# Performance work log

Hardware: AMD Instinct MI355X
Metric: run time of the kernel (lower is better)

Reference implementation:

```python
import jax, jax.numpy as jnp
from jax import lax
import numpy as np

GRID = 8
H384 = 6 * GRID * GRID  # 384, LSTM input and hidden size


def _conv(x, w, b):
    # x: [B,C,H,W], w: [O,I,kh,kw]
    y = lax.conv_general_dilated(x, w, (1, 1), 'VALID',
                                 dimension_numbers=('NCHW', 'OIHW', 'NCHW'))
    return y + b[None, :, None, None]


def _maxpool2(x):
    return lax.reduce_window(x, -jnp.inf, lax.max,
                             (1, 1, 2, 2), (1, 1, 2, 2), 'VALID')


def setup_inputs() -> dict:
    key = jax.random.key(0)
    ks = jax.random.split(key, 20)
    s = 0.05
    d = {
        'x': jax.random.normal(ks[0], (512, 100, 100), jnp.float32),
        # conv stack: Conv2d(1,16,7) ... Conv2d(128,128,3)
        'cw1': jax.random.normal(ks[1], (16, 1, 7, 7), jnp.float32) * s,
        'cb1': jnp.zeros((16,), jnp.float32),
        'cw2': jax.random.normal(ks[2], (32, 16, 4, 4), jnp.float32) * s,
        'cb2': jnp.zeros((32,), jnp.float32),
        'cw3': jax.random.normal(ks[3], (64, 32, 5, 5), jnp.float32) * s,
        'cb3': jnp.zeros((64,), jnp.float32),
        'cw4': jax.random.normal(ks[4], (128, 64, 5, 5), jnp.float32) * s,
        'cb4': jnp.zeros((128,), jnp.float32),
        'cw5': jax.random.normal(ks[5], (128, 128, 5, 5), jnp.float32) * s,
        'cb5': jnp.zeros((128,), jnp.float32),
        'cw6': jax.random.normal(ks[6], (128, 128, 3, 3), jnp.float32) * s,
        'cb6': jnp.zeros((128,), jnp.float32),
        # linear layers: 8192 -> 1024 -> 384, Sigmoid
        'lw1': jax.random.normal(ks[7], (1024, 8192), jnp.float32) * 0.01,
        'lb1': jnp.zeros((1024,), jnp.float32),
        'lw2': jax.random.normal(ks[8], (384, 1024), jnp.float32) * 0.02,
        'lb2': jnp.zeros((384,), jnp.float32),
        # LSTM (input 384, hidden 384, 1 layer), torch gate order i,f,g,o
        'w_ih': jax.random.normal(ks[9], (4 * H384, H384), jnp.float32) * s,
        'w_hh': jax.random.normal(ks[10], (4 * H384, H384), jnp.float32) * s,
        'b_ih': jnp.zeros((4 * H384,), jnp.float32),
        'b_hh': jnp.zeros((4 * H384,), jnp.float32),
    }
    return d


def reference(x, cw1, cb1, cw2, cb2, cw3, cb3, cw4, cb4, cw5, cb5, cw6, cb6,
              lw1, lb1, lw2, lb2, w_ih, w_hh, b_ih, b_hh):
    B = x.shape[0]
    h = x[:, None, :, :]                       # [B,1,100,100]
    h = _maxpool2(jax.nn.relu(_conv(h, cw1, cb1)))   # [B,16,47,47]
    h = _maxpool2(jax.nn.relu(_conv(h, cw2, cb2)))   # [B,32,22,22]
    h = jax.nn.relu(_conv(h, cw3, cb3))              # [B,64,18,18]
    h = jax.nn.relu(_conv(h, cw4, cb4))              # [B,128,14,14]
    h = jax.nn.relu(_conv(h, cw5, cb5))              # [B,128,10,10]
    h = jax.nn.relu(_conv(h, cw6, cb6))              # [B,128,8,8]
    h = h.reshape(B, -1)                             # [B,8192]
    h = h @ lw1.T + lb1                              # [B,1024]
    h = jax.nn.sigmoid(h @ lw2.T + lb2)              # [B,384]

    # Sequential LSTM over the batch dim with carried (h,c) state
    def step(carry, xt):
        hs, cs = carry
        gates = w_ih @ xt + b_ih + w_hh @ hs + b_hh  # [1536]
        i, f, g, o = jnp.split(gates, 4)
        cs = jax.nn.sigmoid(f) * cs + jax.nn.sigmoid(i) * jnp.tanh(g)
        hs = jax.nn.sigmoid(o) * jnp.tanh(cs)
        return (hs, cs), hs

    init = (jnp.zeros((H384,), x.dtype), jnp.zeros((H384,), x.dtype))
    _, ys = lax.scan(step, init, h)                  # [B,384]
    return ys.reshape(B, 6, GRID, GRID)
```

## Files before the change

### kernel.cpp

```cpp
#include <hip/hip_runtime.h>
#include <cstddef>
#include <cstdint>

#define T256 256

typedef __attribute__((ext_vector_type(8))) short bhalf8;
typedef __attribute__((ext_vector_type(4))) float floatx4;

__device__ __forceinline__ ushort f2bf(float f) {
  union { float f; uint32_t u; } v; v.f = f;
  return (ushort)((v.u + 0x7fffu + ((v.u >> 16) & 1u)) >> 16);
}

__device__ __forceinline__ float fsig(float x) {
  return 1.f / (1.f + __expf(-x));
}
__device__ __forceinline__ float ftanh(float x) {
  const float e = __expf(-2.f * fabsf(x));
  const float r = (1.f - e) / (1.f + e);
  return copysignf(r, x);
}

__global__ __launch_bounds__(256) void conv1_pool_k(
    const float* __restrict__ x, const float* __restrict__ w,
    const float* __restrict__ bias, float* __restrict__ out)
{
  __shared__ float img[10000];
  __shared__ float wsm[16 * 49];
  __shared__ float bsm[16];
  const int b = blockIdx.x, tid = threadIdx.x;
  for (int i = tid; i < 10000; i += T256) img[i] = x[(size_t)b * 10000 + i];
  for (int i = tid; i < 16 * 49; i += T256) wsm[i] = w[i];
  if (tid < 16) bsm[tid] = bias[tid];
  __syncthreads();
  for (int p = tid; p < 47 * 47; p += T256) {
    const int py = p / 47, px = p % 47;
    const int iy0 = 2 * py, ix0 = 2 * px;
    float win[8][8];
#pragma unroll
    for (int r = 0; r < 8; ++r)
#pragma unroll
      for (int c = 0; c < 8; ++c)
        win[r][c] = img[(iy0 + r) * 100 + (ix0 + c)];
#pragma unroll 1
    for (int oc = 0; oc < 16; ++oc) {
      float wr[49];
#pragma unroll
      for (int j = 0; j < 49; ++j) wr[j] = wsm[oc * 49 + j];
      float m = 0.f;
#pragma unroll
      for (int dy = 0; dy < 2; ++dy)
#pragma unroll
        for (int dx = 0; dx < 2; ++dx) {
          float s = bsm[oc];
#pragma unroll
          for (int ky = 0; ky < 7; ++ky)
#pragma unroll
            for (int kx = 0; kx < 7; ++kx)
              s += win[dy + ky][dx + kx] * wr[ky * 7 + kx];
          m = fmaxf(m, s);
        }
      out[((size_t)b * 16 + oc) * 2209 + p] = m;
    }
  }
}

__device__ __forceinline__ void wprep_one(
    const float* __restrict__ w, ushort* __restrict__ bswz,
    int IC, int KW, int OC, int idx)
{
  const int NT = OC / 16;
  const int lane = idx & 63;
  const int nt = (idx >> 6) % NT;
  const int ks = idx / (64 * NT);
  const int oc = nt * 16 + (lane & 15);
  const int kb = ks * 32 + (lane >> 4) * 8;
  ushort tmp[8];
#pragma unroll
  for (int j = 0; j < 8; ++j) {
    const int k = kb + j;
    const int ic = k % IC, tap = k / IC;
    tmp[j] = f2bf(w[((size_t)oc * IC + ic) * (KW * KW) + tap]);
  }
  *(bhalf8*)(bswz + (size_t)idx * 8) = *(const bhalf8*)tmp;
}

__global__ __launch_bounds__(256) void wprep_all_k(
    const float* __restrict__ cw2, const float* __restrict__ cw3,
    const float* __restrict__ cw4, const float* __restrict__ cw5,
    const float* __restrict__ cw6,
    ushort* __restrict__ bw2, ushort* __restrict__ bw3,
    ushort* __restrict__ bw4, ushort* __restrict__ bw5,
    ushort* __restrict__ bw6)
{
  int idx = blockIdx.x * 256 + threadIdx.x;
  if (idx < 6400)  { wprep_one(cw3, bw3, 32, 5, 64, idx); return; }
  idx -= 6400;
  if (idx < 25600) { wprep_one(cw4, bw4, 64, 5, 128, idx); return; }
  idx -= 25600;
  if (idx < 51200) { wprep_one(cw5, bw5, 128, 5, 128, idx); return; }
  idx -= 51200;
  if (idx < 18432) { wprep_one(cw6, bw6, 128, 3, 128, idx); return; }
  idx -= 18432;
  if (idx < 1024)  { wprep_one(cw2, bw2, 16, 4, 32, idx); }
}

__global__ __launch_bounds__(256) void wprep_lin_k(
    const float* __restrict__ w, ushort* __restrict__ bswz,
    int Kdim, int NT, int total)
{
  const int idx = blockIdx.x * 256 + threadIdx.x;
  if (idx >= total) return;
  const int lane = idx & 63;
  const int nt = (idx >> 6) % NT;
  const int ks = idx / (64 * NT);
  const int oc = nt * 16 + (lane & 15);
  const int kb = ks * 32 + (lane >> 4) * 8;
  ushort tmp[8];
#pragma unroll
  for (int j = 0; j < 8; ++j) tmp[j] = f2bf(w[(size_t)oc * Kdim + kb + j]);
  *(bhalf8*)(bswz + (size_t)idx * 8) = *(const bhalf8*)tmp;
}

__global__ __launch_bounds__(256) void f2bf_k(
    const float* __restrict__ in, ushort* __restrict__ outv, int n)
{
  const int i = (blockIdx.x * 256 + threadIdx.x) * 4;
  if (i >= n) return;
  const float4 v = *(const float4*)&in[i];
  ushort tmp[4] = {f2bf(v.x), f2bf(v.y), f2bf(v.z), f2bf(v.w)};
  *(uint2*)&outv[i] = *(const uint2*)tmp;
}

__global__ __launch_bounds__(256) void conv2mfma_k(
    const float* __restrict__ in, const ushort* __restrict__ bswz,
    const float* __restrict__ bias, float* __restrict__ out)
{
  constexpr int IC = 16, IH = 47, IW = 47;
  constexpr int NPIX = IH * IW;
  constexpr int ROWU = IC + 8;
  constexpr int KS = 8;
  __shared__ ushort imgT[NPIX * ROWU];
  const int b = blockIdx.x, tid = threadIdx.x;
  const int lane = tid & 63, wv = tid >> 6;

  for (int e = tid; e < IC * NPIX; e += 256) {
    const int ic = e / NPIX, pix = e % NPIX;
    imgT[pix * ROWU + ic] = f2bf(in[((size_t)b * IC + ic) * NPIX + pix]);
  }
  __syncthreads();

  const int col = lane & 15, g = lane >> 4;
  const float b0 = bias[col], b1 = bias[16 + col];

  for (int it = wv; it < 66; it += 4) {
    const int pyp = it / 3, tx = it - pyp * 3;
    int px = tx * 16 + col; px = px < 43 ? px : 43;
    floatx4 acc[2][2];
#pragma unroll
    for (int dy = 0; dy < 2; ++dy)
#pragma unroll
      for (int nt = 0; nt < 2; ++nt) acc[dy][nt] = (floatx4){0.f, 0.f, 0.f, 0.f};

    for (int ks = 0; ks < KS; ++ks) {
      bhalf8 bf[2];
#pragma unroll
      for (int nt = 0; nt < 2; ++nt)
        bf[nt] = *(const bhalf8*)(bswz + ((size_t)(ks * 2 + nt) * 64 + lane) * 8);
      const int kk = ks * 32 + g * 8;
      const int tap = kk >> 4, icb = kk & 15;
      const int ky = tap >> 2, kx = tap & 3;
      bhalf8 af[2];
#pragma unroll
      for (int dy = 0; dy < 2; ++dy)
        af[dy] = *(const bhalf8*)&imgT[((2 * pyp + dy + ky) * IW + px + kx) * ROWU + icb];
#pragma unroll
      for (int dy = 0; dy < 2; ++dy)
#pragma unroll
        for (int nt = 0; nt < 2; ++nt)
          acc[dy][nt] = __builtin_amdgcn_mfma_f32_16x16x32_bf16(
              af[dy], bf[nt], acc[dy][nt], 0, 0, 0);
    }
#pragma unroll
    for (int nt = 0; nt < 2; ++nt) {
      const int oc = nt * 16 + col;
      const float bb = nt ? b1 : b0;
      float vv[4];
#pragma unroll
      for (int i = 0; i < 4; ++i) vv[i] = fmaxf(acc[0][nt][i], acc[1][nt][i]);
#pragma unroll
      for (int q = 0; q < 2; ++q) {
        const int pxp = tx * 8 + g * 2 + q;
        if (pxp < 22) {
          const float v = fmaxf(fmaxf(vv[2 * q], vv[2 * q + 1]) + bb, 0.f);
          out[((size_t)b * 32 + oc) * 484 + pyp * 22 + pxp] = v;
        }
      }
    }
  }
}

template <int IC, int IH, int IW, int KW_, int OC, int MC>
__global__ __launch_bounds__(256) void convmfma_k(
    const float* __restrict__ in, const ushort* __restrict__ bswz,
    const float* __restrict__ bias, float* __restrict__ out)
{
  constexpr int OH = IH - KW_ + 1, OW = IW - KW_ + 1, P = OH * OW;
  constexpr int NPIX = IH * IW;
  constexpr int KS = IC * KW_ * KW_ / 32;
  constexpr int NT = OC / 16;
  constexpr int NPW = NT / 4;
  constexpr int MT = (P + 15) / 16;
  constexpr int ROWU = IC + 8;
  static_assert(NT % 4 == 0 && IC % 32 == 0, "cfg");

  __shared__ ushort imgT[NPIX * ROWU];
  const int b = blockIdx.x, tid = threadIdx.x;
  const int lane = tid & 63, wv = tid >> 6;
  const int icoff = (lane >> 4) * 8;

  for (int e = tid; e < IC * NPIX; e += 256) {
    const int ic = e / NPIX, pix = e % NPIX;
    imgT[pix * ROWU + ic] = f2bf(in[((size_t)b * IC + ic) * NPIX + pix]);
  }
  __syncthreads();

  for (int m0 = 0; m0 < MT; m0 += MC) {
    floatx4 acc[MC][NPW];
#pragma unroll
    for (int mi = 0; mi < MC; ++mi)
#pragma unroll
      for (int nn = 0; nn < NPW; ++nn)
        acc[mi][nn] = (floatx4){0.f, 0.f, 0.f, 0.f};

    int pbase[MC];
#pragma unroll
    for (int mi = 0; mi < MC; ++mi) {
      int p = (m0 + mi) * 16 + (lane & 15);
      p = p < P ? p : P - 1;
      pbase[mi] = ((p / OW) * IW + (p % OW)) * ROWU;
    }

    bhalf8 bcur[NPW];
#pragma unroll
    for (int nn = 0; nn < NPW; ++nn)
      bcur[nn] = *(const bhalf8*)(bswz + ((size_t)(wv * NPW + nn) * 64 + lane) * 8);

    for (int ks = 0; ks < KS; ++ks) {
      bhalf8 bnext[NPW];
      if (ks + 1 < KS) {
#pragma unroll
        for (int nn = 0; nn < NPW; ++nn)
          bnext[nn] = *(const bhalf8*)(bswz +
              ((size_t)((ks + 1) * NT + wv * NPW + nn) * 64 + lane) * 8);
      }
      const int tap = (ks * 32) / IC;
      const int icb = (ks * 32) % IC;
      const int aoff = ((tap / KW_) * IW + (tap % KW_)) * ROWU + icb + icoff;
      bhalf8 af[MC];
#pragma unroll
      for (int mi = 0; mi < MC; ++mi)
        af[mi] = *(const bhalf8*)&imgT[pbase[mi] + aoff];
#pragma unroll
      for (int mi = 0; mi < MC; ++mi)
#pragma unroll
        for (int nn = 0; nn < NPW; ++nn)
          acc[mi][nn] = __builtin_amdgcn_mfma_f32_16x16x32_bf16(
              af[mi], bcur[nn], acc[mi][nn], 0, 0, 0);
      if (ks + 1 < KS) {
#pragma unroll
        for (int nn = 0; nn < NPW; ++nn) bcur[nn] = bnext[nn];
      }
    }
#pragma unroll
    for (int mi = 0; mi < MC; ++mi)
#pragma unroll
      for (int nn = 0; nn < NPW; ++nn) {
        const int oc = (wv * NPW + nn) * 16 + (lane & 15);
#pragma unroll
        for (int i = 0; i < 4; ++i) {
          const int p = (m0 + mi) * 16 + (lane >> 4) * 4 + i;
          if (p < P) {
            const float v = fmaxf(acc[mi][nn][i] + bias[oc], 0.f);
            out[((size_t)b * OC + oc) * P + p] = v;
          }
        }
      }
  }
}

__global__ __launch_bounds__(256) void gemm_bf16_k(
    const ushort* __restrict__ abf, const ushort* __restrict__ bswz,
    const float* __restrict__ bias, float* __restrict__ C,
    int M, int N, int K)
{
  __shared__ ushort As[64][72];
  const int bn = blockIdx.x, bm = blockIdx.y, tid = threadIdx.x;
  const int lane = tid & 63, wv = tid >> 6;
  const int m0 = bm * 64, n0 = bn * 64;
  const int NTg = N / 16;
  const int ntg = bn * 4 + wv;
  floatx4 acc[4];
#pragma unroll
  for (int mt = 0; mt < 4; ++mt) acc[mt] = (floatx4){0.f, 0.f, 0.f, 0.f};

  for (int kc = 0; kc < K / 64; ++kc) {
    __syncthreads();
#pragma unroll
    for (int q = 0; q < 2; ++q) {
      const int id = q * 256 + tid;
      const int row = id >> 3, kcol = (id & 7) * 8;
      *(bhalf8*)&As[row][kcol] =
          *(const bhalf8*)&abf[(size_t)(m0 + row) * K + kc * 64 + kcol];
    }
    __syncthreads();
#pragma unroll
    for (int k2 = 0; k2 < 2; ++k2) {
      const int ks = kc * 2 + k2;
      const bhalf8 bf = *(const bhalf8*)(bswz + ((size_t)(ks * NTg + ntg) * 64 + lane) * 8);
      const int ksub = k2 * 32 + (lane >> 4) * 8;
#pragma unroll
      for (int mt = 0; mt < 4; ++mt) {
        const bhalf8 af = *(const bhalf8*)&As[mt * 16 + (lane & 15)][ksub];
        acc[mt] = __builtin_amdgcn_mfma_f32_16x16x32_bf16(af, bf, acc[mt], 0, 0, 0);
      }
    }
  }
  const int n = n0 + wv * 16 + (lane & 15);
  const float bb = bias[n];
#pragma unroll
  for (int mt = 0; mt < 4; ++mt)
#pragma unroll
    for (int i = 0; i < 4; ++i) {
      const int m = m0 + mt * 16 + (lane >> 4) * 4 + i;
      C[(size_t)m * N + n] = acc[mt][i] + bb;
    }
}

template <int ACT>
__global__ __launch_bounds__(256) void gemm_tn_k(
    const float* __restrict__ A, const float* __restrict__ B,
    const float* __restrict__ b1, const float* __restrict__ b2,
    float* __restrict__ C, int M, int N, int K)
{
  __shared__ float As[32][66];
  __shared__ float Bs[32][36];
  const int bn = blockIdx.x, bm = blockIdx.y, tid = threadIdx.x;
  const int tx = tid & 7, ty = tid >> 3;
  const int m0 = bm * 64, n0 = bn * 32;
  double acc[2][4] = {{0, 0, 0, 0}, {0, 0, 0, 0}};
  for (int k0 = 0; k0 < K; k0 += 32) {
    __syncthreads();
#pragma unroll
    for (int l = 0; l < 8; ++l) {
      int id = tid + l * 256;
      int kk = id & 31, mm = id >> 5;
      As[kk][mm] = A[(size_t)(m0 + mm) * K + (k0 + kk)];
    }
#pragma unroll
    for (int l = 0; l < 4; ++l) {
      int id = tid + l * 256;
      int kk = id & 31, nn = id >> 5;
      Bs[kk][nn] = B[(size_t)(n0 + nn) * K + (k0 + kk)];
    }
    __syncthreads();
    float p[2][4] = {{0.f, 0.f, 0.f, 0.f}, {0.f, 0.f, 0.f, 0.f}};
#pragma unroll
    for (int kk = 0; kk < 32; ++kk) {
      const float2 av = *reinterpret_cast<const float2*>(&As[kk][ty * 2]);
      const float4 bv = *reinterpret_cast<const float4*>(&Bs[kk][tx * 4]);
      p[0][0] += av.x * bv.x; p[0][1] += av.x * bv.y;
      p[0][2] += av.x * bv.z; p[0][3] += av.x * bv.w;
      p[1][0] += av.y * bv.x; p[1][1] += av.y * bv.y;
      p[1][2] += av.y * bv.z; p[1][3] += av.y * bv.w;
    }
#pragma unroll
    for (int i = 0; i < 2; ++i)
#pragma unroll
      for (int j = 0; j < 4; ++j) acc[i][j] += (double)p[i][j];
  }
#pragma unroll
  for (int i = 0; i < 2; ++i) {
    const int m = m0 + ty * 2 + i;
#pragma unroll
    for (int j = 0; j < 4; ++j) {
      const int n = n0 + tx * 4 + j;
      double v = acc[i][j] + (double)b1[n];
      if (b2) v += (double)b2[n];
      if (ACT == 1) v = 1.0 / (1.0 + exp(-v));
      C[(size_t)m * N + n] = (float)v;
    }
  }
}

#define NWG 16
#define CPW 24
__global__ __launch_bounds__(768) void lstm_k(
    const float* __restrict__ gin, const float* __restrict__ whh,
    float* __restrict__ out, unsigned long long* __restrict__ tagged)
{
  __shared__ __align__(16) float hsm[8][52];
  __shared__ float gsum[96];
  const int wg = blockIdx.x, tid = threadIdx.x;
  const int r = tid >> 3, lk = tid & 7;
  const int gq = r / CPW, cl = r % CPW;
  const int grow = gq * 384 + wg * CPW + cl;
  float wreg[48];
  {
    const float* wr = whh + (size_t)grow * 384 + lk * 48;
#pragma unroll
    for (int i = 0; i < 48; ++i) wreg[i] = wr[i];
  }
  float c = 0.f;
  if (tid < 64) __builtin_amdgcn_s_setprio(1);
  __syncthreads();
  for (int t = 0; t < 512; ++t) {
    float g0 = 0.f, g1 = 0.f, g2 = 0.f, g3 = 0.f;
    if (tid < CPW) {
      const int j = wg * CPW + tid;
      g0 = gin[(size_t)t * 1536 + 0 * 384 + j];
      g1 = gin[(size_t)t * 1536 + 1 * 384 + j];
      g2 = gin[(size_t)t * 1536 + 2 * 384 + j];
      g3 = gin[(size_t)t * 1536 + 3 * 384 + j];
    }
    if (tid < 384) {
      float hv;
      if (t == 0) {
        hv = 0.f;
      } else {
        unsigned long long u;
        do {
          u = __hip_atomic_load(&tagged[(size_t)(t - 1) * 384 + tid],
                                __ATOMIC_RELAXED, __HIP_MEMORY_SCOPE_AGENT);
        } while ((unsigned)(u >> 32) != (unsigned)t);
        union { unsigned ui; float f; } cv; cv.ui = (unsigned)u; hv = cv.f;
      }
      hsm[tid / 48][tid % 48] = hv;
    }
    __syncthreads();
    float s = 0.f;
    {
      const float4* hp = (const float4*)&hsm[lk][0];
#pragma unroll
      for (int q = 0; q < 12; ++q) {
        const float4 hv = hp[q];
        s += wreg[4 * q + 0] * hv.x + wreg[4 * q + 1] * hv.y
           + wreg[4 * q + 2] * hv.z + wreg[4 * q + 3] * hv.w;
      }
    }
    s += __shfl_xor(s, 1);
    s += __shfl_xor(s, 2);
    s += __shfl_xor(s, 4);
    if (lk == 0) gsum[r] = s;
    __syncthreads();
    if (tid < CPW) {
      const float gi = gsum[0 * CPW + tid] + g0;
      const float gf = gsum[1 * CPW + tid] + g1;
      const float gg = gsum[2 * CPW + tid] + g2;
      const float go = gsum[3 * CPW + tid] + g3;
      const float si = fsig(gi);
      const float sf = fsig(gf);
      const float so = fsig(go);
      c = sf * c + si * ftanh(gg);
      const float hn = so * ftanh(c);
      const int j = wg * CPW + tid;
      union { float f; unsigned ui; } cv; cv.f = hn;
      const unsigned long long pk = ((unsigned long long)(t + 1) << 32) | cv.ui;
      __hip_atomic_store(&tagged[(size_t)t * 384 + j], pk,
                         __ATOMIC_RELAXED, __HIP_MEMORY_SCOPE_AGENT);
      out[(size_t)t * 384 + j] = hn;
    }
  }
}

extern "C" void kernel_launch(void* const* d_in, const int* in_sizes, int n_in,
                              void* d_out, int out_size, void* d_ws, size_t ws_size,
                              hipStream_t stream)
{
  const float* x   = (const float*)d_in[0];
  const float* cw1 = (const float*)d_in[1];
  const float* cb1 = (const float*)d_in[2];
  const float* cw2 = (const float*)d_in[3];
  const float* cb2 = (const float*)d_in[4];
  const float* cw3 = (const float*)d_in[5];
  const float* cb3 = (const float*)d_in[6];
  const float* cw4 = (const float*)d_in[7];
  const float* cb4 = (const float*)d_in[8];
  const float* cw5 = (const float*)d_in[9];
  const float* cb5 = (const float*)d_in[10];
  const float* cw6 = (const float*)d_in[11];
  const float* cb6 = (const float*)d_in[12];
  const float* lw1 = (const float*)d_in[13];
  const float* lb1 = (const float*)d_in[14];
  const float* lw2 = (const float*)d_in[15];
  const float* lb2 = (const float*)d_in[16];
  const float* wih = (const float*)d_in[17];
  const float* whh = (const float*)d_in[18];
  const float* bih = (const float*)d_in[19];
  const float* bhh = (const float*)d_in[20];
  float* out = (float*)d_out;
  char* ws = (char*)d_ws;

  float* bufA = (float*)(ws);
  float* bufB = (float*)(ws + 72384512);
  float* l1o  = (float*)(ws + 123764736);
  float* x2   = (float*)(ws + 125861888);
  float* gin  = (float*)(ws + 126648320);
  ushort* bw3 = (ushort*)(ws + 123764736);
  ushort* bw4 = (ushort*)(ws + 123764736 + 102400);
  ushort* bw5 = (ushort*)(ws + 123764736 + 512000);
  ushort* bw6 = (ushort*)(ws + 123764736 + 1331200);
  ushort* bw2 = (ushort*)(ws + 123764736 + 1626112);
  ushort* bw1 = (ushort*)(ws);
  ushort* abf = (ushort*)(ws + 16777216);
  unsigned long long* tagged = (unsigned long long*)(ws + 25165824);

  wprep_all_k<<<(102656 + 255) / 256, 256, 0, stream>>>(
      cw2, cw3, cw4, cw5, cw6, bw2, bw3, bw4, bw5, bw6);

  conv1_pool_k<<<512, 256, 0, stream>>>(x, cw1, cb1, bufA);
  conv2mfma_k<<<512, 256, 0, stream>>>(bufA, bw2, cb2, bufB);
  convmfma_k<32, 22, 22, 5, 64, 7><<<512, 256, 0, stream>>>(bufB, bw3, cb3, bufA);
  convmfma_k<64, 18, 18, 5, 128, 7><<<512, 256, 0, stream>>>(bufA, bw4, cb4, bufB);
  convmfma_k<128, 14, 14, 5, 128, 7><<<512, 256, 0, stream>>>(bufB, bw5, cb5, bufA);
  convmfma_k<128, 10, 10, 3, 128, 4><<<512, 256, 0, stream>>>(bufA, bw6, cb6, bufB);
  wprep_lin_k<<<(256 * 64 * 64 + 255) / 256, 256, 0, stream>>>(lw1, bw1, 8192, 64, 256 * 64 * 64);
  f2bf_k<<<(512 * 8192 / 4 + 255) / 256, 256, 0, stream>>>(bufB, abf, 512 * 8192);
  hipMemsetAsync(tagged, 0, 512 * 384 * 8, stream);
  gemm_bf16_k<<<dim3(16, 8), 256, 0, stream>>>(abf, bw1, lb1, l1o, 512, 1024, 8192);
  gemm_tn_k<1><<<dim3(384 / 32, 512 / 64), 256, 0, stream>>>(l1o, lw2, lb2, nullptr, x2, 512, 384, 1024);
  gemm_tn_k<0><<<dim3(1536 / 32, 512 / 64), 256, 0, stream>>>(x2, wih, bih, bhh, gin, 512, 1536, 384);
  lstm_k<<<NWG, 768, 0, stream>>>(gin, whh, out, tagged);
}
```

Before: 1.428 ms.

## Move small linear GEMMs to bf16 MFMA and fuse fp32-to-bf16 conversion

Replaces the fp32/double-accumulating SIMT GEMMs for the 1024->384 linear layer and the LSTM input projection with the bf16 MFMA GEMM. Weight swizzling for all three linear weights is merged into one prep kernel. The activation fp32->bf16 conversion moves into the GEMM's shared-memory load, which removes the separate f2bf pass and its intermediate buffer. The LSTM dot product is also split into two accumulators for more ILP. In exchange, these layers now run at bf16 precision where they previously accumulated in double.

```diff
diff --git a/kernel.cpp b/kernel.cpp
--- a/kernel.cpp
+++ b/kernel.cpp
@@ -105,12 +105,10 @@
   if (idx < 1024)  { wprep_one(cw2, bw2, 16, 4, 32, idx); }
 }
 
-__global__ __launch_bounds__(256) void wprep_lin_k(
+__device__ __forceinline__ void wprep_lin_one(
     const float* __restrict__ w, ushort* __restrict__ bswz,
-    int Kdim, int NT, int total)
-{
-  const int idx = blockIdx.x * 256 + threadIdx.x;
-  if (idx >= total) return;
+    int Kdim, int NT, int idx)
+{
   const int lane = idx & 63;
   const int nt = (idx >> 6) % NT;
   const int ks = idx / (64 * NT);
@@ -122,14 +120,18 @@
   *(bhalf8*)(bswz + (size_t)idx * 8) = *(const bhalf8*)tmp;
 }
 
-__global__ __launch_bounds__(256) void f2bf_k(
-    const float* __restrict__ in, ushort* __restrict__ outv, int n)
-{
-  const int i = (blockIdx.x * 256 + threadIdx.x) * 4;
-  if (i >= n) return;
-  const float4 v = *(const float4*)&in[i];
-  ushort tmp[4] = {f2bf(v.x), f2bf(v.y), f2bf(v.z), f2bf(v.w)};
-  *(uint2*)&outv[i] = *(const uint2*)tmp;
+__global__ __launch_bounds__(256) void wprep_lin3_k(
+    const float* __restrict__ lw1, const float* __restrict__ lw2,
+    const float* __restrict__ wih,
+    ushort* __restrict__ bw1, ushort* __restrict__ bwl2,
+    ushort* __restrict__ bwih)
+{
+  int idx = blockIdx.x * 256 + threadIdx.x;
+  if (idx < 1048576) { wprep_lin_one(lw1, bw1, 8192, 64, idx); return; }
+  idx -= 1048576;
+  if (idx < 49152)   { wprep_lin_one(lw2, bwl2, 1024, 24, idx); return; }
+  idx -= 49152;
+  if (idx < 73728)   { wprep_lin_one(wih, bwih, 384, 96, idx); }
 }
 
 __global__ __launch_bounds__(256) void conv2mfma_k(
@@ -289,10 +291,11 @@
   }
 }
 
+template <int ACT>
 __global__ __launch_bounds__(256) void gemm_bf16_k(
-    const ushort* __restrict__ abf, const ushort* __restrict__ bswz,
-    const float* __restrict__ bias, float* __restrict__ C,
-    int M, int N, int K)
+    const float* __restrict__ A, const ushort* __restrict__ bswz,
+    const float* __restrict__ b1, const float* __restrict__ b2,
+    float* __restrict__ C, int M, int N, int K)
 {
   __shared__ ushort As[64][72];
   const int bn = blockIdx.x, bm = blockIdx.y, tid = threadIdx.x;
@@ -310,8 +313,12 @@
     for (int q = 0; q < 2; ++q) {
       const int id = q * 256 + tid;
       const int row = id >> 3, kcol = (id & 7) * 8;
-      *(bhalf8*)&As[row][kcol] =
-          *(const bhalf8*)&abf[(size_t)(m0 + row) * K + kc * 64 + kcol];
+      const float* ap = &A[(size_t)(m0 + row) * K + kc * 64 + kcol];
+      const float4 v0 = *(const float4*)ap;
+      const float4 v1 = *(const float4*)(ap + 4);
+      ushort t[8] = {f2bf(v0.x), f2bf(v0.y), f2bf(v0.z), f2bf(v0.w),
+                     f2bf(v1.x), f2bf(v1.y), f2bf(v1.z), f2bf(v1.w)};
+      *(bhalf8*)&As[row][kcol] = *(const bhalf8*)t;
     }
     __syncthreads();
 #pragma unroll
@@ -327,70 +334,16 @@
     }
   }
   const int n = n0 + wv * 16 + (lane & 15);
-  const float bb = bias[n];
+  const float bb = b1[n] + (b2 ? b2[n] : 0.f);
 #pragma unroll
   for (int mt = 0; mt < 4; ++mt)
 #pragma unroll
     for (int i = 0; i < 4; ++i) {
       const int m = m0 + mt * 16 + (lane >> 4) * 4 + i;
-      C[(size_t)m * N + n] = acc[mt][i] + bb;
-    }
-}
-
-template <int ACT>
-__global__ __launch_bounds__(256) void gemm_tn_k(
-    const float* __restrict__ A, const float* __restrict__ B,
-    const float* __restrict__ b1, const float* __restrict__ b2,
-    float* __restrict__ C, int M, int N, int K)
-{
-  __shared__ float As[32][66];
-  __shared__ float Bs[32][36];
-  const int bn = blockIdx.x, bm = blockIdx.y, tid = threadIdx.x;
-  const int tx = tid & 7, ty = tid >> 3;
-  const int m0 = bm * 64, n0 = bn * 32;
-  double acc[2][4] = {{0, 0, 0, 0}, {0, 0, 0, 0}};
-  for (int k0 = 0; k0 < K; k0 += 32) {
-    __syncthreads();
-#pragma unroll
-    for (int l = 0; l < 8; ++l) {
-      int id = tid + l * 256;
-      int kk = id & 31, mm = id >> 5;
-      As[kk][mm] = A[(size_t)(m0 + mm) * K + (k0 + kk)];
-    }
-#pragma unroll
-    for (int l = 0; l < 4; ++l) {
-      int id = tid + l * 256;
-      int kk = id & 31, nn = id >> 5;
-      Bs[kk][nn] = B[(size_t)(n0 + nn) * K + (k0 + kk)];
-    }
-    __syncthreads();
-    float p[2][4] = {{0.f, 0.f, 0.f, 0.f}, {0.f, 0.f, 0.f, 0.f}};
-#pragma unroll
-    for (int kk = 0; kk < 32; ++kk) {
-      const float2 av = *reinterpret_cast<const float2*>(&As[kk][ty * 2]);
-      const float4 bv = *reinterpret_cast<const float4*>(&Bs[kk][tx * 4]);
-      p[0][0] += av.x * bv.x; p[0][1] += av.x * bv.y;
-      p[0][2] += av.x * bv.z; p[0][3] += av.x * bv.w;
-      p[1][0] += av.y * bv.x; p[1][1] += av.y * bv.y;
-      p[1][2] += av.y * bv.z; p[1][3] += av.y * bv.w;
-    }
-#pragma unroll
-    for (int i = 0; i < 2; ++i)
-#pragma unroll
-      for (int j = 0; j < 4; ++j) acc[i][j] += (double)p[i][j];
-  }
-#pragma unroll
-  for (int i = 0; i < 2; ++i) {
-    const int m = m0 + ty * 2 + i;
-#pragma unroll
-    for (int j = 0; j < 4; ++j) {
-      const int n = n0 + tx * 4 + j;
-      double v = acc[i][j] + (double)b1[n];
-      if (b2) v += (double)b2[n];
-      if (ACT == 1) v = 1.0 / (1.0 + exp(-v));
-      C[(size_t)m * N + n] = (float)v;
-    }
-  }
+      float v = acc[mt][i] + bb;
+      if (ACT == 1) v = 1.f / (1.f + expf(-v));
+      C[(size_t)m * N + n] = v;
+    }
 }
 
 #define NWG 16
@@ -438,16 +391,19 @@
       hsm[tid / 48][tid % 48] = hv;
     }
     __syncthreads();
-    float s = 0.f;
+    float s0 = 0.f, s1 = 0.f;
     {
       const float4* hp = (const float4*)&hsm[lk][0];
 #pragma unroll
-      for (int q = 0; q < 12; ++q) {
-        const float4 hv = hp[q];
-        s += wreg[4 * q + 0] * hv.x + wreg[4 * q + 1] * hv.y
-           + wreg[4 * q + 2] * hv.z + wreg[4 * q + 3] * hv.w;
-      }
-    }
+      for (int q = 0; q < 12; q += 2) {
+        const float4 ha = hp[q], hb = hp[q + 1];
+        s0 += wreg[4 * q + 0] * ha.x + wreg[4 * q + 1] * ha.y
+            + wreg[4 * q + 2] * ha.z + wreg[4 * q + 3] * ha.w;
+        s1 += wreg[4 * q + 4] * hb.x + wreg[4 * q + 5] * hb.y
+            + wreg[4 * q + 6] * hb.z + wreg[4 * q + 7] * hb.w;
+      }
+    }
+    float s = s0 + s1;
     s += __shfl_xor(s, 1);
     s += __shfl_xor(s, 2);
     s += __shfl_xor(s, 4);
@@ -511,9 +467,10 @@
   ushort* bw5 = (ushort*)(ws + 123764736 + 512000);
   ushort* bw6 = (ushort*)(ws + 123764736 + 1331200);
   ushort* bw2 = (ushort*)(ws + 123764736 + 1626112);
-  ushort* bw1 = (ushort*)(ws);
-  ushort* abf = (ushort*)(ws + 16777216);
+  ushort* bw1  = (ushort*)(ws);
   unsigned long long* tagged = (unsigned long long*)(ws + 25165824);
+  ushort* bwl2 = (ushort*)(ws + 26738688);
+  ushort* bwih = (ushort*)(ws + 27525120);
 
   wprep_all_k<<<(102656 + 255) / 256, 256, 0, stream>>>(
       cw2, cw3, cw4, cw5, cw6, bw2, bw3, bw4, bw5, bw6);
@@ -524,11 +481,11 @@
   convmfma_k<64, 18, 18, 5, 128, 7><<<512, 256, 0, stream>>>(bufA, bw4, cb4, bufB);
   convmfma_k<128, 14, 14, 5, 128, 7><<<512, 256, 0, stream>>>(bufB, bw5, cb5, bufA);
   convmfma_k<128, 10, 10, 3, 128, 4><<<512, 256, 0, stream>>>(bufA, bw6, cb6, bufB);
-  wprep_lin_k<<<(256 * 64 * 64 + 255) / 256, 256, 0, stream>>>(lw1, bw1, 8192, 64, 256 * 64 * 64);
-  f2bf_k<<<(512 * 8192 / 4 + 255) / 256, 256, 0, stream>>>(bufB, abf, 512 * 8192);
+  wprep_lin3_k<<<(1171456 + 255) / 256, 256, 0, stream>>>(
+      lw1, lw2, wih, bw1, bwl2, bwih);
   hipMemsetAsync(tagged, 0, 512 * 384 * 8, stream);
-  gemm_bf16_k<<<dim3(16, 8), 256, 0, stream>>>(abf, bw1, lb1, l1o, 512, 1024, 8192);
-  gemm_tn_k<1><<<dim3(384 / 32, 512 / 64), 256, 0, stream>>>(l1o, lw2, lb2, nullptr, x2, 512, 384, 1024);
-  gemm_tn_k<0><<<dim3(1536 / 32, 512 / 64), 256, 0, stream>>>(x2, wih, bih, bhh, gin, 512, 1536, 384);
+  gemm_bf16_k<0><<<dim3(16, 8), 256, 0, stream>>>(bufB, bw1, lb1, nullptr, l1o, 512, 1024, 8192);
+  gemm_bf16_k<1><<<dim3(6, 8), 256, 0, stream>>>(l1o, bwl2, lb2, nullptr, x2, 512, 384, 1024);
+  gemm_bf16_k<0><<<dim3(24, 8), 256, 0, stream>>>(x2, bwih, bih, bhh, gin, 512, 1536, 384);
   lstm_k<<<NWG, 768, 0, stream>>>(gin, whh, out, tagged);
 }
```

Result: no change. 1.421 ms (-0.5%).
